# Performance work log

Measured on AMD Instinct MI355X. Metric: run time of the kernel, lower is better.

Reference implementation:

```python
import jax, jax.numpy as jnp
import numpy as np

B, N, IN, OUT = 16, 1000, 128, 128


def setup_inputs() -> dict:
    key = jax.random.key(0)
    ks = jax.random.split(key, 8)
    stdv = 1.0 / np.sqrt(IN + OUT)  # matches reset_param uniform(-stdv, stdv)
    def w(k):
        return jax.random.uniform(k, (N, IN + OUT, OUT), jnp.float32, -stdv, stdv)
    return {
        "xt": jax.random.normal(ks[0], (B, N, IN), jnp.float32),
        "hidden": jax.random.normal(ks[1], (1, N, OUT), jnp.float32),
        "ct_1": jax.random.normal(ks[2], (1, N, OUT), jnp.float32),
        "W_i": w(ks[3]), "b_i": jnp.zeros((N, OUT), jnp.float32),
        "W_o": w(ks[4]), "b_o": jnp.zeros((N, OUT), jnp.float32),
        "W_f": w(ks[5]), "b_f": jnp.zeros((N, OUT), jnp.float32),
        "W_c": w(ks[6]), "b_c": jnp.zeros((N, OUT), jnp.float32),
    }


def reference(xt, hidden, ct_1, W_i, b_i, W_o, b_o, W_f, b_f, W_c, b_c):
    b = xt.shape[0]
    h = jnp.broadcast_to(hidden, (b,) + hidden.shape[1:])       # [B,N,OUT]
    xh = jnp.concatenate([xt, h], axis=-1)                      # [B,N,IN+OUT]

    def gate(W, bias, act):
        # per-stock batched matmul: [B,N,K] x [N,K,O] -> [B,N,O]
        return act(jnp.einsum('bnk,nko->bno', xh, W) + bias)

    it = gate(W_i, b_i, jax.nn.sigmoid)
    ot = gate(W_o, b_o, jax.nn.sigmoid)
    ft = gate(W_f, b_f, jax.nn.sigmoid)
    chat = gate(W_c, b_c, jnp.tanh)

    ct = ft * jnp.broadcast_to(ct_1, it.shape) + it * chat
    ht = ot * jnp.tanh(ct)
    return ht, ct
```

## Files before the change

kernel.cpp:

```cpp
#include <hip/hip_runtime.h>
#include <hip/hip_bf16.h>

namespace {
constexpr int B   = 16;
constexpr int NS  = 1000;
constexpr int IN  = 128;
constexpr int OUT = 128;
constexpr int K   = 256;

typedef __attribute__((ext_vector_type(8))) short short8;
typedef __attribute__((ext_vector_type(4))) float f32x4;

__device__ __forceinline__ float fsigmoid(float x) {
  return 1.0f / (1.0f + __expf(-x));
}
__device__ __forceinline__ float ftanh(float x) {
  return 2.0f / (1.0f + __expf(-2.0f * x)) - 1.0f;
}
__device__ __forceinline__ unsigned int f2bf(float f) {
  unsigned int u = __builtin_bit_cast(unsigned int, f);
  u += 0x7fffu + ((u >> 16) & 1u);
  return u >> 16;
}
__device__ __forceinline__ unsigned int pack2(float lo, float hi) {
  return f2bf(lo) | (f2bf(hi) << 16);
}

__global__ __launch_bounds__(512, 6) void lstm_kernel(
    const float* __restrict__ xt, const float* __restrict__ hidden,
    const float* __restrict__ ct_1,
    const float* __restrict__ Wi, const float* __restrict__ bi,
    const float* __restrict__ Wo, const float* __restrict__ bo,
    const float* __restrict__ Wf, const float* __restrict__ bfp,
    const float* __restrict__ Wc, const float* __restrict__ bc,
    float* __restrict__ out) {
  __shared__ __align__(16) unsigned char smem[33024];

  const int n   = blockIdx.x;
  const int tid = threadIdx.x;

  {
    const int b  = tid >> 5;
    const int s  = tid & 31;
    const int k0 = s << 3;
    float v[8];
    if (k0 < IN) {
      const float4 a = *reinterpret_cast<const float4*>(xt + ((size_t)b * NS + n) * IN + k0);
      const float4 c = *reinterpret_cast<const float4*>(xt + ((size_t)b * NS + n) * IN + k0 + 4);
      v[0]=a.x; v[1]=a.y; v[2]=a.z; v[3]=a.w; v[4]=c.x; v[5]=c.y; v[6]=c.z; v[7]=c.w;
    } else {
      const float4 a = *reinterpret_cast<const float4*>(hidden + (size_t)n * OUT + (k0 - IN));
      const float4 c = *reinterpret_cast<const float4*>(hidden + (size_t)n * OUT + (k0 - IN) + 4);
      v[0]=a.x; v[1]=a.y; v[2]=a.z; v[3]=a.w; v[4]=c.x; v[5]=c.y; v[6]=c.z; v[7]=c.w;
    }
    uint4 pk;
    pk.x = pack2(v[0], v[1]); pk.y = pack2(v[2], v[3]);
    pk.z = pack2(v[4], v[5]); pk.w = pack2(v[6], v[7]);
    const int addr = ((b << 9) + (s << 4)) ^ ((b & 7) << 4);
    *reinterpret_cast<uint4*>(&smem[addr]) = pk;
  }
  __syncthreads();

  const int wid  = tid >> 6;
  const int g    = wid >> 1;
  const int half = wid & 1;
  const int l    = tid & 63;
  const int g2   = l >> 4;
  const int c16  = l & 15;

  const float* Wg = (g == 0) ? Wi : (g == 1) ? Wo : (g == 2) ? Wf : Wc;
  const float* bg = (g == 0) ? bi : (g == 1) ? bo : (g == 2) ? bfp : bc;
  const float* wq = Wg + (size_t)n * (K * OUT) + (size_t)(g2 << 3) * OUT + half * 64 + c16;

  f32x4 acc[4] = {f32x4{0,0,0,0}, f32x4{0,0,0,0}, f32x4{0,0,0,0}, f32x4{0,0,0,0}};

  #pragma unroll 1
  for (int c = 0; c < 8; ++c) {
    float w[4][8];
    #pragma unroll
    for (int t = 0; t < 4; ++t)
      #pragma unroll
      for (int j = 0; j < 8; ++j)
        w[t][j] = wq[(j << 7) + (t << 4)];
    wq += 32 * OUT;

    const int aaddr = ((c16 << 9) + (c << 6) + (g2 << 4)) ^ ((c16 & 7) << 4);
    const short8 af = *reinterpret_cast<const short8*>(&smem[aaddr]);

    #pragma unroll
    for (int t = 0; t < 4; ++t) {
      uint4 bu;
      bu.x = pack2(w[t][0], w[t][1]);
      bu.y = pack2(w[t][2], w[t][3]);
      bu.z = pack2(w[t][4], w[t][5]);
      bu.w = pack2(w[t][6], w[t][7]);
      const short8 bfv = __builtin_bit_cast(short8, bu);
      acc[t] = __builtin_amdgcn_mfma_f32_16x16x32_bf16(af, bfv, acc[t], 0, 0, 0);
    }
  }

  __syncthreads();
  float* gb = reinterpret_cast<float*>(smem);
  #pragma unroll
  for (int t = 0; t < 4; ++t) {
    const int colg = (half << 6) + (t << 4) + c16;
    const float bias = bg[(size_t)n * OUT + colg];
    #pragma unroll
    for (int r = 0; r < 4; ++r) {
      const int b = (g2 << 2) + r;
      gb[g * 2064 + b * 129 + colg] = acc[t][r] + bias;
    }
  }
  __syncthreads();

  const size_t nbase = (size_t)n * OUT;
  #pragma unroll
  for (int r = 0; r < 4; ++r) {
    const int p = tid + (r << 9);
    const int b = p >> 7;
    const int o = p & 127;
    const float gi = gb[0 * 2064 + b * 129 + o];
    const float go = gb[1 * 2064 + b * 129 + o];
    const float gf = gb[2 * 2064 + b * 129 + o];
    const float gc = gb[3 * 2064 + b * 129 + o];
    const float it = fsigmoid(gi);
    const float ot = fsigmoid(go);
    const float ft = fsigmoid(gf);
    const float ch = ftanh(gc);
    const float cp = ct_1[nbase + o];
    const float ct = ft * cp + it * ch;
    const float ht = ot * ftanh(ct);
    const size_t oidx = (size_t)b * ((size_t)NS * OUT) + nbase + o;
    out[oidx] = ht;
    out[(size_t)B * NS * OUT + oidx] = ct;
  }
}
}

extern "C" void kernel_launch(void* const* d_in, const int* in_sizes, int n_in,
                              void* d_out, int out_size, void* d_ws, size_t ws_size,
                              hipStream_t stream) {
  const float* xt     = (const float*)d_in[0];
  const float* hidden = (const float*)d_in[1];
  const float* ct_1   = (const float*)d_in[2];
  const float* Wi     = (const float*)d_in[3];
  const float* bi     = (const float*)d_in[4];
  const float* Wo     = (const float*)d_in[5];
  const float* bo     = (const float*)d_in[6];
  const float* Wf     = (const float*)d_in[7];
  const float* bf     = (const float*)d_in[8];
  const float* Wc     = (const float*)d_in[9];
  const float* bc     = (const float*)d_in[10];

  lstm_kernel<<<NS, 512, 0, stream>>>(xt, hidden, ct_1, Wi, bi, Wo, bo,
                                      Wf, bf, Wc, bc,
                                      (float*)d_out);
}
```

Measured before the change: 109.6 us.

## Stream weights through LDS with async global_load_lds and double-issue prefetch

Replaces the direct per-element global loads of weights with async global_load_lds into per-wave LDS buffers. Each chunk is staged one iteration ahead so weight loads overlap the MFMA work. The A operand now comes straight from global memory per lane and is converted to bf16 in registers, which removes the upfront smem staging of xt/hidden and its barrier. LDS grows to 64KB and occupancy bounds drop to 4 blocks, and there is only a single buffer per wave, with reuse guarded by waitcnts.

```diff
diff --git a/kernel.cpp b/kernel.cpp
--- a/kernel.cpp
+++ b/kernel.cpp
@@ -26,7 +26,7 @@
   return f2bf(lo) | (f2bf(hi) << 16);
 }
 
-__global__ __launch_bounds__(512, 6) void lstm_kernel(
+__global__ __launch_bounds__(512, 4) void lstm_kernel(
     const float* __restrict__ xt, const float* __restrict__ hidden,
     const float* __restrict__ ct_1,
     const float* __restrict__ Wi, const float* __restrict__ bi,
@@ -34,33 +34,10 @@
     const float* __restrict__ Wf, const float* __restrict__ bfp,
     const float* __restrict__ Wc, const float* __restrict__ bc,
     float* __restrict__ out) {
-  __shared__ __align__(16) unsigned char smem[33024];
+  __shared__ __align__(16) unsigned char smem[65536];
 
   const int n   = blockIdx.x;
   const int tid = threadIdx.x;
-
-  {
-    const int b  = tid >> 5;
-    const int s  = tid & 31;
-    const int k0 = s << 3;
-    float v[8];
-    if (k0 < IN) {
-      const float4 a = *reinterpret_cast<const float4*>(xt + ((size_t)b * NS + n) * IN + k0);
-      const float4 c = *reinterpret_cast<const float4*>(xt + ((size_t)b * NS + n) * IN + k0 + 4);
-      v[0]=a.x; v[1]=a.y; v[2]=a.z; v[3]=a.w; v[4]=c.x; v[5]=c.y; v[6]=c.z; v[7]=c.w;
-    } else {
-      const float4 a = *reinterpret_cast<const float4*>(hidden + (size_t)n * OUT + (k0 - IN));
-      const float4 c = *reinterpret_cast<const float4*>(hidden + (size_t)n * OUT + (k0 - IN) + 4);
-      v[0]=a.x; v[1]=a.y; v[2]=a.z; v[3]=a.w; v[4]=c.x; v[5]=c.y; v[6]=c.z; v[7]=c.w;
-    }
-    uint4 pk;
-    pk.x = pack2(v[0], v[1]); pk.y = pack2(v[2], v[3]);
-    pk.z = pack2(v[4], v[5]); pk.w = pack2(v[6], v[7]);
-    const int addr = ((b << 9) + (s << 4)) ^ ((b & 7) << 4);
-    *reinterpret_cast<uint4*>(&smem[addr]) = pk;
-  }
-  __syncthreads();
-
   const int wid  = tid >> 6;
   const int g    = wid >> 1;
   const int half = wid & 1;
@@ -70,33 +47,73 @@
 
   const float* Wg = (g == 0) ? Wi : (g == 1) ? Wo : (g == 2) ? Wf : Wc;
   const float* bg = (g == 0) ? bi : (g == 1) ? bo : (g == 2) ? bfp : bc;
-  const float* wq = Wg + (size_t)n * (K * OUT) + (size_t)(g2 << 3) * OUT + half * 64 + c16;
+
+  unsigned char* wbuf = smem + (wid << 13);
+  const float* wcb = Wg + (size_t)n * (K * OUT) + half * 64;
+
+  auto stage_chunk = [&](int r) {
+    #pragma unroll
+    for (int i = 0; i < 8; ++i) {
+      const int cq = (c16 + ((i >> 1) << 2)) & 15;
+      const float* src =
+          wcb + (size_t)((r << 5) + (i << 2) + g2) * OUT + (cq << 2);
+      __builtin_amdgcn_global_load_lds(
+          (const __attribute__((address_space(1))) void*)src,
+          (__attribute__((address_space(3))) void*)(wbuf + (i << 10)),
+          16, 0, 0);
+    }
+  };
+  auto load_a = [&](int r, float4& x0, float4& x1) {
+    const int k = (r << 5) + (g2 << 3);
+    const float* s = (k < IN) ? (xt + ((size_t)c16 * NS + n) * IN + k)
+                              : (hidden + (size_t)n * OUT + (k - IN));
+    x0 = *reinterpret_cast<const float4*>(s);
+    x1 = *reinterpret_cast<const float4*>(s + 4);
+  };
 
   f32x4 acc[4] = {f32x4{0,0,0,0}, f32x4{0,0,0,0}, f32x4{0,0,0,0}, f32x4{0,0,0,0}};
 
+  stage_chunk(0);
+  float4 a0, a1;
+  load_a(0, a0, a1);
+
   #pragma unroll 1
-  for (int c = 0; c < 8; ++c) {
-    float w[4][8];
+  for (int r = 0; r < 8; ++r) {
+    asm volatile("s_waitcnt vmcnt(0)" ::: "memory");
+
+    float wv[4][8];
     #pragma unroll
-    for (int t = 0; t < 4; ++t)
+    for (int t = 0; t < 4; ++t) {
+      const int pb = (((((t << 2) + (c16 >> 2)) - (g2 << 2)) & 15) << 4) +
+                     ((c16 & 3) << 2);
       #pragma unroll
       for (int j = 0; j < 8; ++j)
-        w[t][j] = wq[(j << 7) + (t << 4)];
-    wq += 32 * OUT;
+        wv[t][j] = *reinterpret_cast<const float*>(
+            wbuf + (g2 << 11) + (j << 8) + pb);
+    }
+    uint4 au;
+    au.x = pack2(a0.x, a0.y); au.y = pack2(a0.z, a0.w);
+    au.z = pack2(a1.x, a1.y); au.w = pack2(a1.z, a1.w);
+    const short8 af = __builtin_bit_cast(short8, au);
 
-    const int aaddr = ((c16 << 9) + (c << 6) + (g2 << 4)) ^ ((c16 & 7) << 4);
-    const short8 af = *reinterpret_cast<const short8*>(&smem[aaddr]);
+    asm volatile("s_waitcnt lgkmcnt(0)" ::: "memory");
+    float4 na0 = a0, na1 = a1;
+    if (r < 7) {
+      stage_chunk(r + 1);
+      load_a(r + 1, na0, na1);
+    }
 
     #pragma unroll
     for (int t = 0; t < 4; ++t) {
       uint4 bu;
-      bu.x = pack2(w[t][0], w[t][1]);
-      bu.y = pack2(w[t][2], w[t][3]);
-      bu.z = pack2(w[t][4], w[t][5]);
-      bu.w = pack2(w[t][6], w[t][7]);
-      const short8 bfv = __builtin_bit_cast(short8, bu);
-      acc[t] = __builtin_amdgcn_mfma_f32_16x16x32_bf16(af, bfv, acc[t], 0, 0, 0);
+      bu.x = pack2(wv[t][0], wv[t][1]);
+      bu.y = pack2(wv[t][2], wv[t][3]);
+      bu.z = pack2(wv[t][4], wv[t][5]);
+      bu.w = pack2(wv[t][6], wv[t][7]);
+      acc[t] = __builtin_amdgcn_mfma_f32_16x16x32_bf16(
+          af, __builtin_bit_cast(short8, bu), acc[t], 0, 0, 0);
     }
+    a0 = na0; a1 = na1;
   }
 
   __syncthreads();
@@ -106,9 +123,9 @@
     const int colg = (half << 6) + (t << 4) + c16;
     const float bias = bg[(size_t)n * OUT + colg];
     #pragma unroll
-    for (int r = 0; r < 4; ++r) {
-      const int b = (g2 << 2) + r;
-      gb[g * 2064 + b * 129 + colg] = acc[t][r] + bias;
+    for (int r2 = 0; r2 < 4; ++r2) {
+      const int b = (g2 << 2) + r2;
+      gb[g * 2064 + b * 129 + colg] = acc[t][r2] + bias;
     }
   }
   __syncthreads();
```

Result: no change. 108.0 us (-1.5%).
